# Optimization experiments

Measured on AMD Instinct MI355X. Metric: run time of the kernel, lower is better.

## Reference

```python
import jax, jax.numpy as jnp
import numpy as np

B, K, C, L = 16, 8, 64, 2048
OFFSET = 2.0  # self.offset in Coupling
EPS = 1e-7    # clamp for logit stability (flows' safe_log analogue)


def setup_inputs() -> dict:
    key = jax.random.key(0)
    ks = jax.random.split(key, 6)
    return {
        "x_change": jax.random.normal(ks[0], (B, C, L), jnp.float32),
        "a": jax.random.normal(ks[1], (B, C, L), jnp.float32),
        "b": jax.random.normal(ks[2], (B, C, L), jnp.float32),
        "pi": jax.random.normal(ks[3], (B, K, C, L), jnp.float32),
        "mu": jax.random.normal(ks[4], (B, K, C, L), jnp.float32),
        "s": jax.random.normal(ks[5], (B, K, C, L), jnp.float32) * 0.1,  # log-scales
        "sldj": jnp.zeros((B,), jnp.float32),
    }


def reference(x_change, a, b, pi, mu, s, sldj):
    # scale = sigmoid(a + offset) + (1 - sigmoid(offset))
    sig_off = 1.0 - jax.nn.sigmoid(jnp.float32(OFFSET))
    scale = jax.nn.sigmoid(a + OFFSET) + sig_off                      # [B,C,L]

    logpi = jax.nn.log_softmax(pi, axis=1)                            # [B,K,C,L]
    z = (x_change[:, None] - mu) * jnp.exp(-s)                        # [B,K,C,L]

    # logistic.mixture_log_cdf: logsumexp_k(log pi_k + log sigmoid(z_k))
    log_cdf = jax.scipy.special.logsumexp(logpi + jax.nn.log_sigmoid(z), axis=1)
    u = jnp.clip(jnp.exp(log_cdf), EPS, 1.0 - EPS)                    # [B,C,L]

    # logistic.inverse (forward): logit, with ldj = -log(u) - log(1-u)
    y = jnp.log(u) - jnp.log1p(-u)
    scale_ldj = -jnp.log(u) - jnp.log1p(-u)

    # logistic.mixture_log_pdf: logsumexp_k(log pi_k + z - s - 2 softplus(z))
    log_pdf = jax.scipy.special.logsumexp(
        logpi + z - s - 2.0 * jax.nn.softplus(z), axis=1)             # [B,C,L]

    sldj_out = sldj + jnp.sum(
        (log_pdf + scale_ldj + jnp.log(scale)).reshape(sldj.shape[0], -1), axis=-1)
    out = (y + b) * scale                                             # [B,C,L]
    return out, sldj_out
```

## Files before the change

### kernel.cpp

```cpp
#include <hip/hip_runtime.h>
#include <stdint.h>

#define BB 16
#define KK 8
#define CC 64
#define LL 2048

constexpr int CL = CC * LL;
constexpr int NELEM = BB * CL;
constexpr int TILE = 256;
constexpr int NBLOCKS = NELEM / TILE;
constexpr int NSTREAM = 27;

#define SIG_OFF 0.11920292202211755f
#define LOG_EPS -16.11809565095832f

__device__ __forceinline__ float frcp(float x) { return __builtin_amdgcn_rcpf(x); }

__device__ __forceinline__ void load_to_lds16(const float* g, float* l) {
    __builtin_amdgcn_global_load_lds(
        (const __attribute__((address_space(1))) void*)g,
        (__attribute__((address_space(3))) void*)l,
        16, 0, 0);
}

__global__ void init_sldj_kernel(const float* __restrict__ sldj_in,
                                 float* __restrict__ sldj_out) {
    int i = threadIdx.x;
    if (i < BB) sldj_out[i] = sldj_in[i];
}

__global__ __launch_bounds__(256) void coupling_kernel(
    const float* __restrict__ x,
    const float* __restrict__ a,
    const float* __restrict__ bv,
    const float* __restrict__ pi,
    const float* __restrict__ mu,
    const float* __restrict__ s,
    float* __restrict__ out,
    float* __restrict__ sldj_out) {

    __shared__ float lds[NSTREAM * TILE];

    const int tile = blockIdx.x;
    const int b    = tile >> 9;
    const int base = tile * TILE;
    const int rem  = base & (CL - 1);
    const int kb0  = (b << 20) + rem;

    const int lane = threadIdx.x & 63;
    const int wv   = threadIdx.x >> 6;

    for (int sidx = wv; sidx < NSTREAM; sidx += 4) {
        const float* gp;
        if (sidx == 0)       gp = x  + base;
        else if (sidx == 1)  gp = a  + base;
        else if (sidx == 2)  gp = bv + base;
        else if (sidx < 11)  gp = pi + kb0 + (sidx - 3)  * CL;
        else if (sidx < 19)  gp = mu + kb0 + (sidx - 11) * CL;
        else                 gp = s  + kb0 + (sidx - 19) * CL;
        load_to_lds16(gp + lane * 4, &lds[sidx * TILE + lane * 4]);
    }
    __syncthreads();

    const int t  = threadIdx.x;
    const float xe = lds[0 * TILE + t];
    const float ae = lds[1 * TILE + t];
    const float be = lds[2 * TILE + t];

    float Spi = 0.f, Nc = 0.f, N1 = 0.f, Np = 0.f;

#pragma unroll
    for (int k = 0; k < KK; ++k) {
        const float p  = lds[(3 + k)  * TILE + t];
        const float m  = lds[(11 + k) * TILE + t];
        const float sk = lds[(19 + k) * TILE + t];

        const float invstd = __expf(-sk);
        const float z      = (xe - m) * invstd;

        const float tt = __expf(-fabsf(z));
        const float r  = frcp(1.f + tt);
        const float tr = tt * r;
        const float sig  = (z >= 0.f) ? r  : tr;
        const float osig = (z >= 0.f) ? tr : r;

        const float ek = __expf(p);
        Spi += ek;
        Nc  += ek * sig;
        N1  += ek * osig;
        Np  += ek * invstd * sig * osig;
    }

    const float lSpi = __logf(Spi);
    const float lu   = fmaxf(__logf(Nc) - lSpi, LOG_EPS);
    const float lomu = fmaxf(__logf(N1) - lSpi, LOG_EPS);
    const float y        = lu - lomu;
    const float ldj_term = -lu - lomu;
    const float log_pdf  = __logf(Np) - lSpi;

    const float av = ae + 2.f;
    const float t2 = __expf(-fabsf(av));
    const float r2 = frcp(1.f + t2);
    const float sc = ((av >= 0.f) ? r2 : t2 * r2) + SIG_OFF;

    out[base + t] = (y + be) * sc;

    float contrib = log_pdf + ldj_term + __logf(sc);

#pragma unroll
    for (int off = 32; off > 0; off >>= 1)
        contrib += __shfl_down(contrib, off, 64);

    __shared__ float wsum[4];
    if (lane == 0) wsum[wv] = contrib;
    __syncthreads();
    if (threadIdx.x == 0) {
        atomicAdd(&sldj_out[b], wsum[0] + wsum[1] + wsum[2] + wsum[3]);
    }
}

extern "C" void kernel_launch(void* const* d_in, const int* in_sizes, int n_in,
                              void* d_out, int out_size, void* d_ws, size_t ws_size,
                              hipStream_t stream) {
    const float* x    = (const float*)d_in[0];
    const float* a    = (const float*)d_in[1];
    const float* bv   = (const float*)d_in[2];
    const float* pi   = (const float*)d_in[3];
    const float* mu   = (const float*)d_in[4];
    const float* s    = (const float*)d_in[5];
    const float* sldj = (const float*)d_in[6];

    float* out      = (float*)d_out;
    float* sldj_out = out + (size_t)NELEM;

    init_sldj_kernel<<<1, 64, 0, stream>>>(sldj, sldj_out);
    coupling_kernel<<<NBLOCKS, 256, 0, stream>>>(x, a, bv, pi, mu, s, out, sldj_out);
}
```

Before: 265.0 us.

## Enlarge tiles and double-buffer per-component mixture loads through LDS

Result: faster. 228.0 us (-14.0%).

```diff
diff --git a/kernel.cpp b/kernel.cpp
--- a/kernel.cpp
+++ b/kernel.cpp
@@ -1,5 +1,4 @@
 #include <hip/hip_runtime.h>
-#include <stdint.h>
 
 #define BB 16
 #define KK 8
@@ -8,9 +7,9 @@
 
 constexpr int CL = CC * LL;
 constexpr int NELEM = BB * CL;
-constexpr int TILE = 256;
+constexpr int TILE = 2048;
 constexpr int NBLOCKS = NELEM / TILE;
-constexpr int NSTREAM = 27;
+constexpr int TPB = 256;
 
 #define SIG_OFF 0.11920292202211755f
 #define LOG_EPS -16.11809565095832f
@@ -40,73 +39,119 @@
     float* __restrict__ out,
     float* __restrict__ sldj_out) {
 
-    __shared__ float lds[NSTREAM * TILE];
+    __shared__ float xab[3 * TILE];
+    __shared__ float kbuf[2][3 * TILE];
 
-    const int tile = blockIdx.x;
-    const int b    = tile >> 9;
-    const int base = tile * TILE;
+    const int blk  = blockIdx.x;
+    const int b    = blk >> 6;
+    const int base = blk * TILE;
     const int rem  = base & (CL - 1);
     const int kb0  = (b << 20) + rem;
 
-    const int lane = threadIdx.x & 63;
-    const int wv   = threadIdx.x >> 6;
+    const int tid  = threadIdx.x;
+    const int lane = tid & 63;
+    const int wv   = tid >> 6;
+    const int l4   = lane * 4;
 
-    for (int sidx = wv; sidx < NSTREAM; sidx += 4) {
-        const float* gp;
-        if (sidx == 0)       gp = x  + base;
-        else if (sidx == 1)  gp = a  + base;
-        else if (sidx == 2)  gp = bv + base;
-        else if (sidx < 11)  gp = pi + kb0 + (sidx - 3)  * CL;
-        else if (sidx < 19)  gp = mu + kb0 + (sidx - 11) * CL;
-        else                 gp = s  + kb0 + (sidx - 19) * CL;
-        load_to_lds16(gp + lane * 4, &lds[sidx * TILE + lane * 4]);
+#pragma unroll
+    for (int j = 0; j < 6; ++j) {
+        const int i  = wv * 6 + j;
+        const int st = i >> 3;
+        const int ch = i & 7;
+        const float* gp = (st == 0 ? x : st == 1 ? a : bv) + base + ch * 256 + l4;
+        load_to_lds16(gp, &xab[st * TILE + ch * 256 + l4]);
+    }
+#pragma unroll
+    for (int j = 0; j < 6; ++j) {
+        const int i  = wv * 6 + j;
+        const int st = i >> 3;
+        const int ch = i & 7;
+        const float* gp = (st == 0 ? pi : st == 1 ? mu : s) + kb0 + ch * 256 + l4;
+        load_to_lds16(gp, &kbuf[0][st * TILE + ch * 256 + l4]);
     }
     __syncthreads();
 
-    const int t  = threadIdx.x;
-    const float xe = lds[0 * TILE + t];
-    const float ae = lds[1 * TILE + t];
-    const float be = lds[2 * TILE + t];
+    float4 x4[2];
+    x4[0] = *(const float4*)&xab[0 * TILE + 4 * tid];
+    x4[1] = *(const float4*)&xab[0 * TILE + 1024 + 4 * tid];
 
-    float Spi = 0.f, Nc = 0.f, N1 = 0.f, Np = 0.f;
+    float Spi[8] = {0,0,0,0,0,0,0,0};
+    float Nc [8] = {0,0,0,0,0,0,0,0};
+    float N1 [8] = {0,0,0,0,0,0,0,0};
+    float Np [8] = {0,0,0,0,0,0,0,0};
 
+    for (int k = 0; k < KK; ++k) {
+        const int cur = k & 1;
+        if (k + 1 < KK) {
 #pragma unroll
-    for (int k = 0; k < KK; ++k) {
-        const float p  = lds[(3 + k)  * TILE + t];
-        const float m  = lds[(11 + k) * TILE + t];
-        const float sk = lds[(19 + k) * TILE + t];
-
-        const float invstd = __expf(-sk);
-        const float z      = (xe - m) * invstd;
-
-        const float tt = __expf(-fabsf(z));
-        const float r  = frcp(1.f + tt);
-        const float tr = tt * r;
-        const float sig  = (z >= 0.f) ? r  : tr;
-        const float osig = (z >= 0.f) ? tr : r;
-
-        const float ek = __expf(p);
-        Spi += ek;
-        Nc  += ek * sig;
-        N1  += ek * osig;
-        Np  += ek * invstd * sig * osig;
+            for (int j = 0; j < 6; ++j) {
+                const int i  = wv * 6 + j;
+                const int st = i >> 3;
+                const int ch = i & 7;
+                const float* gp = (st == 0 ? pi : st == 1 ? mu : s)
+                                  + kb0 + (k + 1) * CL + ch * 256 + l4;
+                load_to_lds16(gp, &kbuf[1 - cur][st * TILE + ch * 256 + l4]);
+            }
+        }
+#pragma unroll
+        for (int g = 0; g < 2; ++g) {
+            const float4 p4 = *(const float4*)&kbuf[cur][0 * TILE + g * 1024 + 4 * tid];
+            const float4 m4 = *(const float4*)&kbuf[cur][1 * TILE + g * 1024 + 4 * tid];
+            const float4 s4 = *(const float4*)&kbuf[cur][2 * TILE + g * 1024 + 4 * tid];
+            const float xs[4] = {g ? x4[1].x : x4[0].x, g ? x4[1].y : x4[0].y,
+                                 g ? x4[1].z : x4[0].z, g ? x4[1].w : x4[0].w};
+            const float ps[4] = {p4.x, p4.y, p4.z, p4.w};
+            const float ms[4] = {m4.x, m4.y, m4.z, m4.w};
+            const float ss[4] = {s4.x, s4.y, s4.z, s4.w};
+#pragma unroll
+            for (int e = 0; e < 4; ++e) {
+                const int ei = g * 4 + e;
+                const float invstd = __expf(-ss[e]);
+                const float z      = (xs[e] - ms[e]) * invstd;
+                const float tt = __expf(-fabsf(z));
+                const float r  = frcp(1.f + tt);
+                const float tr = tt * r;
+                const float sig  = (z >= 0.f) ? r  : tr;
+                const float osig = (z >= 0.f) ? tr : r;
+                const float ek = __expf(ps[e]);
+                Spi[ei] += ek;
+                Nc [ei] += ek * sig;
+                N1 [ei] += ek * osig;
+                Np [ei] += ek * invstd * sig * osig;
+            }
+        }
+        __syncthreads();
     }
 
-    const float lSpi = __logf(Spi);
-    const float lu   = fmaxf(__logf(Nc) - lSpi, LOG_EPS);
-    const float lomu = fmaxf(__logf(N1) - lSpi, LOG_EPS);
-    const float y        = lu - lomu;
-    const float ldj_term = -lu - lomu;
-    const float log_pdf  = __logf(Np) - lSpi;
+    float contrib = 0.f;
+#pragma unroll
+    for (int g = 0; g < 2; ++g) {
+        const float4 a4 = *(const float4*)&xab[1 * TILE + g * 1024 + 4 * tid];
+        const float4 b4 = *(const float4*)&xab[2 * TILE + g * 1024 + 4 * tid];
+        const float as[4] = {a4.x, a4.y, a4.z, a4.w};
+        const float bs[4] = {b4.x, b4.y, b4.z, b4.w};
+        float4 o4;
+        float* op = (float*)&o4;
+#pragma unroll
+        for (int e = 0; e < 4; ++e) {
+            const int ei = g * 4 + e;
+            const float lSpi = __logf(Spi[ei]);
+            const float lu   = fmaxf(__logf(Nc[ei]) - lSpi, LOG_EPS);
+            const float lomu = fmaxf(__logf(N1[ei]) - lSpi, LOG_EPS);
+            const float y        = lu - lomu;
+            const float ldj_term = -lu - lomu;
+            const float log_pdf  = __logf(Np[ei]) - lSpi;
 
-    const float av = ae + 2.f;
-    const float t2 = __expf(-fabsf(av));
-    const float r2 = frcp(1.f + t2);
-    const float sc = ((av >= 0.f) ? r2 : t2 * r2) + SIG_OFF;
+            const float av = as[e] + 2.f;
+            const float t2 = __expf(-fabsf(av));
+            const float r2 = frcp(1.f + t2);
+            const float sc = ((av >= 0.f) ? r2 : t2 * r2) + SIG_OFF;
 
-    out[base + t] = (y + be) * sc;
-
-    float contrib = log_pdf + ldj_term + __logf(sc);
+            op[e] = (y + bs[e]) * sc;
+            contrib += log_pdf + ldj_term + __logf(sc);
+        }
+        *(float4*)(out + base + g * 1024 + 4 * tid) = o4;
+    }
 
 #pragma unroll
     for (int off = 32; off > 0; off >>= 1)
@@ -115,7 +160,7 @@
     __shared__ float wsum[4];
     if (lane == 0) wsum[wv] = contrib;
     __syncthreads();
-    if (threadIdx.x == 0) {
+    if (tid == 0) {
         atomicAdd(&sldj_out[b], wsum[0] + wsum[1] + wsum[2] + wsum[3]);
     }
 }
@@ -135,5 +180,5 @@
     float* sldj_out = out + (size_t)NELEM;
 
     init_sldj_kernel<<<1, 64, 0, stream>>>(sldj, sldj_out);
-    coupling_kernel<<<NBLOCKS, 256, 0, stream>>>(x, a, bv, pi, mu, s, out, sldj_out);
+    coupling_kernel<<<NBLOCKS, TPB, 0, stream>>>(x, a, bv, pi, mu, s, out, sldj_out);
 }
```
